# Performance work log

Hardware: AMD Instinct MI355X
Metric: run time of the kernel (lower is better)

The kernel has to match this reference:

```python
import jax, jax.numpy as jnp
import numpy as np

N = 50000
E = 800000
DIM = 256
HEADS = 4
HDIM = DIM // HEADS  # 64
NEG_SLOPE = 0.2
LN_EPS = 1e-5


def _layernorm(x, g, b):
    mu = jnp.mean(x, axis=-1, keepdims=True)
    var = jnp.var(x, axis=-1, keepdims=True)
    return (x - mu) * jax.lax.rsqrt(var + LN_EPS) * g + b


def setup_inputs() -> dict:
    key = jax.random.key(0)
    ks = jax.random.split(key, 10)
    x = jax.random.normal(ks[0], (N, DIM), dtype=jnp.float32)
    edge_index = jax.random.randint(ks[1], (2, E), 0, N, dtype=jnp.int64)
    s = 0.05
    W = jax.random.normal(ks[2], (DIM, DIM), dtype=jnp.float32) * s       # GAT linear (heads*out = dim)
    a_src = jax.random.normal(ks[3], (HEADS, HDIM), dtype=jnp.float32) * s
    a_dst = jax.random.normal(ks[4], (HEADS, HDIM), dtype=jnp.float32) * s
    gat_b = jnp.zeros((DIM,), dtype=jnp.float32)
    ln_g = jnp.ones((DIM,), dtype=jnp.float32)
    ln_b = jnp.zeros((DIM,), dtype=jnp.float32)
    W1 = jax.random.normal(ks[5], (DIM, 4 * DIM), dtype=jnp.float32) * s
    b1 = jnp.zeros((4 * DIM,), dtype=jnp.float32)
    W2 = jax.random.normal(ks[6], (4 * DIM, DIM), dtype=jnp.float32) * s
    b2 = jnp.zeros((DIM,), dtype=jnp.float32)
    return {"x": x, "edge_index": edge_index, "W": W, "a_src": a_src,
            "a_dst": a_dst, "gat_b": gat_b, "ln_g": ln_g, "ln_b": ln_b,
            "W1": W1, "b1": b1, "W2": W2, "b2": b2}


def _gat(x, edge_index, W, a_src, a_dst, gat_b):
    # project and split heads: [N, H, C]
    h = (x @ W).reshape(N, HEADS, HDIM)
    alpha_src = jnp.einsum('nhc,hc->nh', h, a_src)  # [N, H]
    alpha_dst = jnp.einsum('nhc,hc->nh', h, a_dst)  # [N, H]
    src = edge_index[0]
    dst = edge_index[1]
    e = jax.nn.leaky_relu(alpha_src[src] + alpha_dst[dst], NEG_SLOPE)  # [E, H]
    # segment softmax over edges sharing a destination node
    m = jax.ops.segment_max(e, dst, num_segments=N)                   # [N, H]
    ex = jnp.exp(e - m[dst])
    denom = jax.ops.segment_sum(ex, dst, num_segments=N)              # [N, H]
    alpha = ex / (denom[dst] + 1e-16)                                 # [E, H]
    msg = h[src] * alpha[:, :, None]                                  # [E, H, C]
    out = jax.ops.segment_sum(msg.reshape(E, DIM), dst, num_segments=N)
    return out + gat_b


def reference(x, edge_index, W, a_src, a_dst, gat_b, ln_g, ln_b, W1, b1, W2, b2):
    residual = x
    g = _gat(x, edge_index, W, a_src, a_dst, gat_b)
    x = _layernorm(x + g, ln_g, ln_b)
    ffn = jax.nn.gelu(x @ W1 + b1, approximate=False) @ W2 + b2
    x = _layernorm(x + ffn, ln_g, ln_b)  # same norm params reused, as in source
    return x + residual
```

## Files before the change

kernel.cpp:

```cpp
#include <hip/hip_runtime.h>
#include <hip/hip_bf16.h>
#include <math.h>

typedef __bf16 bf16;
typedef bf16 bf16x8 __attribute__((ext_vector_type(8)));
typedef float floatx4 __attribute__((ext_vector_type(4)));

#define NN 50000
#define EE 800000
#define DIMC 256
#define FFC 1024

typedef __attribute__((address_space(3))) unsigned int lds_u32;
typedef __attribute__((address_space(1))) unsigned int gbl_u32;

static __device__ __forceinline__ void glds16(const bf16* g, bf16* l) {
    __builtin_amdgcn_global_load_lds((const gbl_u32*)g, (lds_u32*)l, 16, 0, 0);
}

static __device__ __forceinline__ unsigned short f2b(float f) {
    bf16 b = (bf16)f;
    return __builtin_bit_cast(unsigned short, b);
}
static __device__ __forceinline__ float b2f_lo(unsigned u) { return __uint_as_float(u << 16); }
static __device__ __forceinline__ float b2f_hi(unsigned u) { return __uint_as_float(u & 0xffff0000u); }

static __device__ __forceinline__ float gelu_f(float v) {
    float z = -1.5957691216f * v - 0.0713548163f * v * v * v;
    return v / (1.f + __expf(z));
}

__global__ __launch_bounds__(256)
void k_cast_count(const float* __restrict__ in, bf16* __restrict__ out, long n4,
                  const int* __restrict__ dst, unsigned* __restrict__ deg) {
    long i = (long)blockIdx.x * 256 + threadIdx.x;
    if (i < EE) atomicAdd(&deg[dst[(int)i]], 1u);
    if (i >= n4) return;
    float4 v = ((const float4*)in)[i];
    uint2 p;
    p.x = (unsigned)f2b(v.x) | ((unsigned)f2b(v.y) << 16);
    p.y = (unsigned)f2b(v.z) | ((unsigned)f2b(v.w) << 16);
    ((uint2*)out)[i] = p;
}

__global__ __launch_bounds__(256)
void k_tcast_all(const float* __restrict__ W, bf16* __restrict__ WT,
                 const float* __restrict__ W1, bf16* __restrict__ W1T,
                 const float* __restrict__ W2, bf16* __restrict__ W2T) {
    __shared__ float t[32][33];
    int b = blockIdx.x;
    const float* in; bf16* out; int K, Nc, bx, by;
    if (b < 64)        { in = W;  out = WT;  K = 256;  Nc = 256;  bx = b & 7;  by = b >> 3; }
    else if (b < 320)  { b -= 64;  in = W1; out = W1T; K = 256;  Nc = 1024; bx = b & 31; by = b >> 5; }
    else               { b -= 320; in = W2; out = W2T; K = 1024; Nc = 256;  bx = b & 7;  by = b >> 3; }
    int n0 = bx * 32, k0 = by * 32;
    int tx = threadIdx.x & 31, ty = threadIdx.x >> 5;
#pragma unroll
    for (int i = 0; i < 4; ++i)
        t[ty + i * 8][tx] = in[(long)(k0 + ty + i * 8) * Nc + n0 + tx];
    __syncthreads();
#pragma unroll
    for (int i = 0; i < 4; ++i)
        out[(long)(n0 + ty + i * 8) * K + k0 + tx] = (bf16)t[tx][ty + i * 8];
}

template <int EPI>
__global__ __launch_bounds__(256)
void k_gemmA(const bf16* __restrict__ A, const bf16* __restrict__ BT,
             bf16* __restrict__ C, const float* __restrict__ bias,
             const float* __restrict__ avs, const float* __restrict__ avd,
             float* __restrict__ asrcO, float* __restrict__ adstO,
             int M, int K, int Nc) {
    __shared__ __attribute__((aligned(16))) bf16 smem[17408];
    bf16* As = smem;
    bf16* Bs = smem + 8192;
    const int tid = threadIdx.x;
    const int w = tid >> 6, lane = tid & 63;
    const int gm = blockIdx.x * 128, gn = blockIdx.y * 128;
    const int wm = (w >> 1) * 64, wn = (w & 1) * 64;
    const int lr = lane & 15, lkc = lane >> 4;

    long aoff[4], boff[4];
#pragma unroll
    for (int j = 0; j < 4; ++j) {
        int s = w * 4 + j;
        int r = s * 8 + (lane >> 3);
        int kc = ((lane & 7) ^ (r & 7)) * 8;
        aoff[j] = (long)min(gm + r, M - 1) * K + kc;
        boff[j] = (long)(gn + r) * K + kc;
    }

    floatx4 acc[4][4];
#pragma unroll
    for (int a = 0; a < 4; ++a)
#pragma unroll
        for (int b = 0; b < 4; ++b) acc[a][b] = floatx4{0.f, 0.f, 0.f, 0.f};

    for (int k0 = 0; k0 < K; k0 += 64) {
        if (k0) __syncthreads();
#pragma unroll
        for (int j = 0; j < 4; ++j) {
            int s = w * 4 + j;
            glds16(A + aoff[j] + k0, As + s * 512);
            glds16(BT + boff[j] + k0, Bs + s * 512);
        }
        __syncthreads();
#pragma unroll
        for (int kk = 0; kk < 2; ++kk) {
            bf16x8 af[4], bv[4];
#pragma unroll
            for (int mi = 0; mi < 4; ++mi) {
                int r = wm + mi * 16 + lr;
                int ch = (kk * 4 + lkc) ^ (r & 7);
                af[mi] = *(const bf16x8*)(As + r * 64 + ch * 8);
            }
#pragma unroll
            for (int ni = 0; ni < 4; ++ni) {
                int r = wn + ni * 16 + lr;
                int ch = (kk * 4 + lkc) ^ (r & 7);
                bv[ni] = *(const bf16x8*)(Bs + r * 64 + ch * 8);
            }
#pragma unroll
            for (int mi = 0; mi < 4; ++mi)
#pragma unroll
                for (int ni = 0; ni < 4; ++ni)
                    acc[mi][ni] = __builtin_amdgcn_mfma_f32_16x16x32_bf16(af[mi], bv[ni], acc[mi][ni], 0, 0, 0);
        }
    }

    __syncthreads();
    bf16* cs = smem;
#pragma unroll
    for (int ni = 0; ni < 4; ++ni) {
        const int cl = wn + ni * 16 + lr;
        const float bvs = (EPI == 1) ? bias[gn + cl] : 0.f;
#pragma unroll
        for (int mi = 0; mi < 4; ++mi)
#pragma unroll
            for (int i = 0; i < 4; ++i) {
                int rl = wm + mi * 16 + lkc * 4 + i;
                float v = acc[mi][ni][i] + bvs;
                if (EPI == 1) v = gelu_f(v);
                cs[rl * 136 + cl] = (bf16)v;
            }
    }
    __syncthreads();

    const int c8 = (lane & 15) * 8;
    float as8[8], ad8[8];
    int hd = 0;
    if (EPI == 0) {
        hd = (gn >> 6) + ((lane & 15) >> 3);
        const int cb = hd * 64 + (c8 & 63);
#pragma unroll
        for (int i = 0; i < 8; ++i) { as8[i] = avs[cb + i]; ad8[i] = avd[cb + i]; }
    }

#pragma unroll
    for (int t = 0; t < 8; ++t) {
        int rl = w * 32 + t * 4 + (lane >> 4);
        int grow = gm + rl;
        uint4 val = *(const uint4*)(cs + rl * 136 + c8);
        if (grow < M) *(uint4*)(C + (long)grow * Nc + gn + c8) = val;
        if (EPI == 0) {
            float h0 = b2f_lo(val.x), h1 = b2f_hi(val.x), h2 = b2f_lo(val.y), h3 = b2f_hi(val.y);
            float h4 = b2f_lo(val.z), h5 = b2f_hi(val.z), h6 = b2f_lo(val.w), h7 = b2f_hi(val.w);
            float ds = h0 * as8[0] + h1 * as8[1] + h2 * as8[2] + h3 * as8[3]
                     + h4 * as8[4] + h5 * as8[5] + h6 * as8[6] + h7 * as8[7];
            float dd = h0 * ad8[0] + h1 * ad8[1] + h2 * ad8[2] + h3 * ad8[3]
                     + h4 * ad8[4] + h5 * ad8[5] + h6 * ad8[6] + h7 * ad8[7];
#pragma unroll
            for (int off = 1; off < 8; off <<= 1) { ds += __shfl_xor(ds, off); dd += __shfl_xor(dd, off); }
            if ((lane & 7) == 0 && grow < M) {
                asrcO[grow * 4 + hd] = ds;
                adstO[grow * 4 + hd] = dd;
            }
        }
    }
}

__global__ __launch_bounds__(512)
void k_ffn(const bf16* __restrict__ x1b, const bf16* __restrict__ W1T,
           const bf16* __restrict__ W2T, const float* __restrict__ b1,
           const float* __restrict__ b2, const float* __restrict__ x,
           const float* __restrict__ lng, const float* __restrict__ lnb,
           float* __restrict__ out, int M) {
    __shared__ __attribute__((aligned(16))) bf16 smem[20480];
    float* actf = (float*)smem;
    bf16* w1s = smem + 4096;
    bf16* w2s = smem + 12288;
    const int tid = threadIdx.x;
    const int w = tid >> 6, lane = tid & 63;
    const int lr = lane & 15, lkc = lane >> 4;
    const int mg = w >> 1, nh = w & 1;
    const int gm = blockIdx.x * 64;

    bf16x8 xf[8];
    {
        long rb = (long)min(gm + mg * 16 + lr, M - 1) * DIMC;
#pragma unroll
        for (int kf = 0; kf < 8; ++kf)
            xf[kf] = *(const bf16x8*)(x1b + rb + kf * 32 + lkc * 8);
    }

    floatx4 accB[8];
#pragma unroll
    for (int i = 0; i < 8; ++i) accB[i] = floatx4{0.f, 0.f, 0.f, 0.f};

    const int rbA = nh * 16 + lr;
    const int rAct = mg * 16 + lr;
    const int kAct = nh * 16 + lr;

    for (int c = 0; c < 32; ++c) {
        if (c) __syncthreads();
#pragma unroll
        for (int j = 0; j < 2; ++j) {
            int sg = w * 2 + j;
            int r = sg * 2 + (lane >> 5);
            int col = ((lane & 31) ^ (r & 7)) * 8;
            glds16(W1T + (long)(c * 32 + r) * DIMC + col, w1s + sg * 512);
        }
#pragma unroll
        for (int j = 0; j < 2; ++j) {
            int sg = w * 2 + j;
            int r = sg * 16 + (lane >> 2);
            int col = c * 32 + (((lane & 3) ^ ((r >> 1) & 3)) * 8);
            glds16(W2T + (long)r * FFC + col, w2s + sg * 512);
        }
        __syncthreads();

        floatx4 a0 = floatx4{0.f, 0.f, 0.f, 0.f}, a1 = a0;
#pragma unroll
        for (int kf = 0; kf < 8; kf += 2) {
            int g0 = (kf * 4 + lkc) ^ (rbA & 7);
            int g1 = ((kf + 1) * 4 + lkc) ^ (rbA & 7);
            bf16x8 bva = *(const bf16x8*)(w1s + rbA * 256 + g0 * 8);
            bf16x8 bvb = *(const bf16x8*)(w1s + rbA * 256 + g1 * 8);
            a0 = __builtin_amdgcn_mfma_f32_16x16x32_bf16(xf[kf], bva, a0, 0, 0, 0);
            a1 = __builtin_amdgcn_mfma_f32_16x16x32_bf16(xf[kf + 1], bvb, a1, 0, 0, 0);
        }
        float b1v = b1[c * 32 + kAct];
#pragma unroll
        for (int i = 0; i < 4; ++i) {
            int r = mg * 16 + lkc * 4 + i;
            float v = gelu_f(a0[i] + a1[i] + b1v);
            actf[r * 32 + (((kAct >> 2) ^ (r & 7)) << 2) + (kAct & 3)] = v;
        }
        __syncthreads();

        {
            int g0 = (lkc * 2) ^ (rAct & 7);
            int g1 = (lkc * 2 + 1) ^ (rAct & 7);
            float4 lo = *(const float4*)(actf + rAct * 32 + g0 * 4);
            float4 hi = *(const float4*)(actf + rAct * 32 + g1 * 4);
            bf16x8 af;
            af[0] = (bf16)lo.x; af[1] = (bf16)lo.y; af[2] = (bf16)lo.z; af[3] = (bf16)lo.w;
            af[4] = (bf16)hi.x; af[5] = (bf16)hi.y; af[6] = (bf16)hi.z; af[7] = (bf16)hi.w;
#pragma unroll
            for (int ni = 0; ni < 8; ++ni) {
                int rb = nh * 128 + ni * 16 + lr;
                int gb = lkc ^ ((rb >> 1) & 3);
                bf16x8 bv = *(const bf16x8*)(w2s + rb * 32 + gb * 8);
                accB[ni] = __builtin_amdgcn_mfma_f32_16x16x32_bf16(af, bv, accB[ni], 0, 0, 0);
            }
        }
    }

    __syncthreads();
    bf16* cs = smem;
#pragma unroll
    for (int ni = 0; ni < 8; ++ni) {
        int col = nh * 128 + ni * 16 + lr;
        float b2v = b2[col];
#pragma unroll
        for (int i = 0; i < 4; ++i) {
            int rl = mg * 16 + lkc * 4 + i;
            cs[rl * 264 + col] = (bf16)(accB[ni][i] + b2v);
        }
    }
    __syncthreads();
    float4 g4 = *(const float4*)(lng + lane * 4);
    float4 lb4 = *(const float4*)(lnb + lane * 4);
#pragma unroll 1
    for (int t = 0; t < 8; ++t) {
        int r = w * 8 + t;
        int grow = gm + r;
        long base = (long)min(grow, M - 1) * DIMC + lane * 4;
        uint2 cu = *(const uint2*)(cs + r * 264 + lane * 4);
        uint2 xu = *(const uint2*)(x1b + base);
        float v0 = b2f_lo(cu.x) + b2f_lo(xu.x);
        float v1 = b2f_hi(cu.x) + b2f_hi(xu.x);
        float v2 = b2f_lo(cu.y) + b2f_lo(xu.y);
        float v3 = b2f_hi(cu.y) + b2f_hi(xu.y);
        float s1 = v0 + v1 + v2 + v3;
        float s2 = v0 * v0 + v1 * v1 + v2 * v2 + v3 * v3;
#pragma unroll
        for (int off = 1; off < 64; off <<= 1) { s1 += __shfl_xor(s1, off); s2 += __shfl_xor(s2, off); }
        float mu = s1 * (1.f / DIMC);
        float rs = rsqrtf(s2 * (1.f / DIMC) - mu * mu + 1e-5f);
        float4 xr = *(const float4*)(x + base);
        float4 o;
        o.x = (v0 - mu) * rs * g4.x + lb4.x + xr.x;
        o.y = (v1 - mu) * rs * g4.y + lb4.y + xr.y;
        o.z = (v2 - mu) * rs * g4.z + lb4.z + xr.z;
        o.w = (v3 - mu) * rs * g4.w + lb4.w + xr.w;
        if (grow < M) *(float4*)(out + (long)grow * DIMC + lane * 4) = o;
    }
}

__global__ __launch_bounds__(1024)
void k_scan1(const unsigned* __restrict__ deg, unsigned* __restrict__ rowoff,
             unsigned* __restrict__ cursor, unsigned* __restrict__ bsum) {
    __shared__ unsigned wsum[16], wscan[16];
    int tid = threadIdx.x, lane = tid & 63, wid = tid >> 6;
    int i = blockIdx.x * 1024 + tid;
    unsigned v = (i < NN) ? deg[i] : 0u;
    unsigned s = v;
    for (int off = 1; off < 64; off <<= 1) {
        unsigned t = __shfl_up(s, off);
        if (lane >= off) s += t;
    }
    if (lane == 63) wsum[wid] = s;
    __syncthreads();
    if (wid == 0) {
        unsigned t = (lane < 16) ? wsum[lane] : 0u;
        unsigned ts = t;
        for (int off = 1; off < 16; off <<= 1) {
            unsigned u2 = __shfl_up(ts, off);
            if (lane >= off) ts += u2;
        }
        if (lane < 16) wscan[lane] = ts;
    }
    __syncthreads();
    unsigned basew = (wid > 0) ? wscan[wid - 1] : 0u;
    unsigned excl = basew + (s - v);
    if (i < NN) { rowoff[i] = excl; cursor[i] = excl; }
    if (tid == 0) bsum[blockIdx.x] = wscan[15];
}

__global__ __launch_bounds__(64)
void k_scan2(unsigned* __restrict__ bsum, unsigned* __restrict__ rowoff) {
    int lane = threadIdx.x;
    unsigned v = (lane < 49) ? bsum[lane] : 0u;
    unsigned s = v;
    for (int off = 1; off < 64; off <<= 1) {
        unsigned t = __shfl_up(s, off);
        if (lane >= off) s += t;
    }
    if (lane < 49) bsum[lane] = s - v;
    if (lane == 48) rowoff[NN] = s;
}

__global__ __launch_bounds__(256)
void k_scan3(const unsigned* __restrict__ bsum, unsigned* __restrict__ rowoff,
             unsigned* __restrict__ cursor) {
    int i = blockIdx.x * 256 + threadIdx.x;
    if (i < NN) {
        unsigned o = bsum[i >> 10];
        rowoff[i] += o;
        cursor[i] += o;
    }
}

__global__ __launch_bounds__(256)
void k_fill(const int* __restrict__ src, const int* __restrict__ dst,
            unsigned* __restrict__ cursor, unsigned* __restrict__ elist) {
    int e = blockIdx.x * 256 + threadIdx.x;
    if (e < EE) {
        unsigned p = atomicAdd(&cursor[dst[e]], 1u);
        elist[p] = (unsigned)src[e];
    }
}

__global__ __launch_bounds__(256)
void k_agg_ln1(const unsigned* __restrict__ rowoff, const unsigned* __restrict__ elist,
               const float* __restrict__ asrc, const float* __restrict__ adst,
               const bf16* __restrict__ hb, const float* __restrict__ x,
               const float* __restrict__ gatb, const float* __restrict__ lng,
               const float* __restrict__ lnb, bf16* __restrict__ x1b) {
    int node = (blockIdx.x * 256 + threadIdx.x) >> 6;
    int lane = threadIdx.x & 63;
    if (node >= NN) return;
    int beg = (int)rowoff[node], end = (int)rowoff[node + 1];
    int head = lane >> 4;
    float ad = adst[node * 4 + head];
    const int c = lane * 4;
    const bf16* hc = hb + c;
    const int bl = lane & 48;

    float dsum = 0.f;
    float a0 = 0.f, a1 = 0.f, a2 = 0.f, a3 = 0.f;

    for (int c0 = beg; c0 < end; c0 += 16) {
        int take = end - c0; if (take > 16) take = 16;
        int jj = c0 + (lane & 15);
        float ex = 0.f; int s = 0;
        if (jj < end) {
            s = (int)elist[jj];
            float e = asrc[s * 4 + head] + ad;
            e = (e > 0.f) ? e : 0.2f * e;
            ex = __expf(e);
        }
        dsum += ex;
        if (take == 16) {
#pragma unroll
            for (int j = 0; j < 16; ++j) {
                float al = __shfl(ex, bl + j);
                int sj = __shfl(s, bl + j);
                uint2 u = *(const uint2*)(hc + (long)sj * DIMC);
                a0 += al * b2f_lo(u.x);
                a1 += al * b2f_hi(u.x);
                a2 += al * b2f_lo(u.y);
                a3 += al * b2f_hi(u.y);
            }
        } else {
            for (int j = 0; j < take; ++j) {
                float al = __shfl(ex, bl + j);
                int sj = __shfl(s, bl + j);
                uint2 u = *(const uint2*)(hc + (long)sj * DIMC);
                a0 += al * b2f_lo(u.x);
                a1 += al * b2f_hi(u.x);
                a2 += al * b2f_lo(u.y);
                a3 += al * b2f_hi(u.y);
            }
        }
    }
    dsum += __shfl_xor(dsum, 1);
    dsum += __shfl_xor(dsum, 2);
    dsum += __shfl_xor(dsum, 4);
    dsum += __shfl_xor(dsum, 8);
    float invd = 1.f / (dsum + 1e-16f);
    a0 *= invd; a1 *= invd; a2 *= invd; a3 *= invd;

    long base = (long)node * DIMC + c;
    float4 xr = *(const float4*)(x + base);
    float4 gb = *(const float4*)(gatb + c);
    float v0 = xr.x + a0 + gb.x;
    float v1 = xr.y + a1 + gb.y;
    float v2 = xr.z + a2 + gb.z;
    float v3 = xr.w + a3 + gb.w;
    float s1 = v0 + v1 + v2 + v3;
    float s2 = v0 * v0 + v1 * v1 + v2 * v2 + v3 * v3;
    for (int off = 1; off < 64; off <<= 1) { s1 += __shfl_xor(s1, off); s2 += __shfl_xor(s2, off); }
    float mu = s1 * (1.f / DIMC);
    float rs = rsqrtf(s2 * (1.f / DIMC) - mu * mu + 1e-5f);
    float4 g4 = *(const float4*)(lng + c);
    float4 b4 = *(const float4*)(lnb + c);
    float y0 = (v0 - mu) * rs * g4.x + b4.x;
    float y1 = (v1 - mu) * rs * g4.y + b4.y;
    float y2 = (v2 - mu) * rs * g4.z + b4.z;
    float y3 = (v3 - mu) * rs * g4.w + b4.w;
    uint2 p;
    p.x = (unsigned)f2b(y0) | ((unsigned)f2b(y1) << 16);
    p.y = (unsigned)f2b(y2) | ((unsigned)f2b(y3) << 16);
    *(uint2*)(x1b + base) = p;
}

extern "C" void kernel_launch(void* const* d_in, const int* in_sizes, int n_in,
                              void* d_out, int out_size, void* d_ws, size_t ws_size,
                              hipStream_t stream) {
    const float* x    = (const float*)d_in[0];
    const int*   ei   = (const int*)d_in[1];
    const float* W    = (const float*)d_in[2];
    const float* a_s  = (const float*)d_in[3];
    const float* a_d  = (const float*)d_in[4];
    const float* gatb = (const float*)d_in[5];
    const float* lng  = (const float*)d_in[6];
    const float* lnb  = (const float*)d_in[7];
    const float* W1   = (const float*)d_in[8];
    const float* b1   = (const float*)d_in[9];
    const float* W2   = (const float*)d_in[10];
    const float* b2   = (const float*)d_in[11];
    float* out = (float*)d_out;
    char* ws = (char*)d_ws;

    bf16*     xb     = (bf16*)(ws + 0L);
    bf16*     hb     = (bf16*)(ws + 25600000L);
    bf16*     x1b    = (bf16*)(ws + 51200000L);
    unsigned* bsum   = (unsigned*)(ws + 76800000L);
    float*    asrc   = (float*)(ws + 179200000L);
    float*    adst   = (float*)(ws + 180000000L);
    unsigned* deg    = (unsigned*)(ws + 180800000L);
    unsigned* cursor = (unsigned*)(ws + 181000192L);
    unsigned* rowoff = (unsigned*)(ws + 181200384L);
    unsigned* elist  = (unsigned*)(ws + 181400832L);
    bf16*     WT     = (bf16*)(ws + 184600832L);
    bf16*     W1T    = (bf16*)(ws + 184731904L);
    bf16*     W2T    = (bf16*)(ws + 185256192L);

    const int* esrc = ei;
    const int* edst = ei + EE;

    hipMemsetAsync(deg, 0, NN * sizeof(unsigned), stream);
    k_cast_count<<<12500, 256, 0, stream>>>(x, xb, (long)NN * DIMC / 4, edst, deg);
    k_tcast_all<<<576, 256, 0, stream>>>(W, WT, W1, W1T, W2, W2T);

    dim3 g1(391, 2);
    k_gemmA<0><<<g1, 256, 0, stream>>>(xb, WT, hb, nullptr, a_s, a_d, asrc, adst, NN, DIMC, DIMC);

    k_scan1<<<49, 1024, 0, stream>>>(deg, rowoff, cursor, bsum);
    k_scan2<<<1, 64, 0, stream>>>(bsum, rowoff);
    k_scan3<<<196, 256, 0, stream>>>(bsum, rowoff, cursor);
    k_fill<<<3125, 256, 0, stream>>>(esrc, edst, cursor, elist);

    k_agg_ln1<<<12500, 256, 0, stream>>>(rowoff, elist, asrc, adst, hb, x, gatb, lng, lnb, x1b);

    k_ffn<<<782, 512, 0, stream>>>(x1b, W1T, W2T, b1, b2, x, lng, lnb, out, NN);
}
```

Before: 442.2 us.

## Double-buffer FFN weight staging and pre-gather source attention scores in CSR fill

The FFN kernel now double-buffers the W1/W2 chunk staging in LDS. It prefetches chunk c+1 with async global-to-LDS loads while computing chunk c, and swaps the second __syncthreads for a waitcnt plus raw barrier. Separately, k_fill writes each edge's four source attention scores into a CSR-ordered float4 array, so the aggregation kernel reads them contiguously instead of gathering asrc by random source index. The costs are more LDS per block (which may lower occupancy of the 512-thread FFN blocks) and an extra 12.8 MB scattered write in k_fill.

```diff
diff --git a/kernel.cpp b/kernel.cpp
--- a/kernel.cpp
+++ b/kernel.cpp
@@ -179,16 +179,33 @@
     }
 }
 
+#define STAGE_W(cc, pp) do {                                                    \
+    bf16* w1d = smem + 4096 + (pp) * 8192;                                      \
+    bf16* w2d = smem + 20480 + (pp) * 8192;                                     \
+    _Pragma("unroll")                                                           \
+    for (int j = 0; j < 2; ++j) {                                               \
+        int sg = w * 2 + j;                                                     \
+        int r = sg * 2 + (lane >> 5);                                           \
+        int col = ((lane & 31) ^ (r & 7)) * 8;                                  \
+        glds16(W1T + (long)((cc) * 32 + r) * DIMC + col, w1d + sg * 512);       \
+    }                                                                           \
+    _Pragma("unroll")                                                           \
+    for (int j = 0; j < 2; ++j) {                                               \
+        int sg = w * 2 + j;                                                     \
+        int r = sg * 16 + (lane >> 2);                                          \
+        int col = (cc) * 32 + (((lane & 3) ^ ((r >> 1) & 3)) * 8);              \
+        glds16(W2T + (long)r * FFC + col, w2d + sg * 512);                      \
+    }                                                                           \
+} while (0)
+
 __global__ __launch_bounds__(512)
 void k_ffn(const bf16* __restrict__ x1b, const bf16* __restrict__ W1T,
            const bf16* __restrict__ W2T, const float* __restrict__ b1,
            const float* __restrict__ b2, const float* __restrict__ x,
            const float* __restrict__ lng, const float* __restrict__ lnb,
            float* __restrict__ out, int M) {
-    __shared__ __attribute__((aligned(16))) bf16 smem[20480];
+    __shared__ __attribute__((aligned(16))) bf16 smem[36864];
     float* actf = (float*)smem;
-    bf16* w1s = smem + 4096;
-    bf16* w2s = smem + 12288;
     const int tid = threadIdx.x;
     const int w = tid >> 6, lane = tid & 63;
     const int lr = lane & 15, lkc = lane >> 4;
@@ -211,23 +228,14 @@
     const int rAct = mg * 16 + lr;
     const int kAct = nh * 16 + lr;
 
+    STAGE_W(0, 0);
+
     for (int c = 0; c < 32; ++c) {
-        if (c) __syncthreads();
-#pragma unroll
-        for (int j = 0; j < 2; ++j) {
-            int sg = w * 2 + j;
-            int r = sg * 2 + (lane >> 5);
-            int col = ((lane & 31) ^ (r & 7)) * 8;
-            glds16(W1T + (long)(c * 32 + r) * DIMC + col, w1s + sg * 512);
-        }
-#pragma unroll
-        for (int j = 0; j < 2; ++j) {
-            int sg = w * 2 + j;
-            int r = sg * 16 + (lane >> 2);
-            int col = c * 32 + (((lane & 3) ^ ((r >> 1) & 3)) * 8);
-            glds16(W2T + (long)r * FFC + col, w2s + sg * 512);
-        }
+        const int p = c & 1;
         __syncthreads();
+        if (c < 31) STAGE_W(c + 1, p ^ 1);
+        bf16* w1s = smem + 4096 + p * 8192;
+        bf16* w2s = smem + 20480 + p * 8192;
 
         floatx4 a0 = floatx4{0.f, 0.f, 0.f, 0.f}, a1 = a0;
 #pragma unroll
@@ -246,7 +254,9 @@
             float v = gelu_f(a0[i] + a1[i] + b1v);
             actf[r * 32 + (((kAct >> 2) ^ (r & 7)) << 2) + (kAct & 3)] = v;
         }
-        __syncthreads();
+        asm volatile("s_waitcnt lgkmcnt(0)" ::: "memory");
+        __builtin_amdgcn_s_barrier();
+        asm volatile("" ::: "memory");
 
         {
             int g0 = (lkc * 2) ^ (rAct & 7);
@@ -364,17 +374,20 @@
 
 __global__ __launch_bounds__(256)
 void k_fill(const int* __restrict__ src, const int* __restrict__ dst,
-            unsigned* __restrict__ cursor, unsigned* __restrict__ elist) {
+            const float* __restrict__ asrc, unsigned* __restrict__ cursor,
+            unsigned* __restrict__ elist, float4* __restrict__ evals) {
     int e = blockIdx.x * 256 + threadIdx.x;
     if (e < EE) {
+        int s = src[e];
         unsigned p = atomicAdd(&cursor[dst[e]], 1u);
-        elist[p] = (unsigned)src[e];
+        elist[p] = (unsigned)s;
+        evals[p] = *(const float4*)(asrc + (long)s * 4);
     }
 }
 
 __global__ __launch_bounds__(256)
 void k_agg_ln1(const unsigned* __restrict__ rowoff, const unsigned* __restrict__ elist,
-               const float* __restrict__ asrc, const float* __restrict__ adst,
+               const float* __restrict__ evals, const float* __restrict__ adst,
                const bf16* __restrict__ hb, const float* __restrict__ x,
                const float* __restrict__ gatb, const float* __restrict__ lng,
                const float* __restrict__ lnb, bf16* __restrict__ x1b) {
@@ -397,7 +410,7 @@
         float ex = 0.f; int s = 0;
         if (jj < end) {
             s = (int)elist[jj];
-            float e = asrc[s * 4 + head] + ad;
+            float e = evals[(long)jj * 4 + head] + ad;
             e = (e > 0.f) ? e : 0.2f * e;
             ex = __expf(e);
         }
@@ -478,6 +491,7 @@
     bf16*     hb     = (bf16*)(ws + 25600000L);
     bf16*     x1b    = (bf16*)(ws + 51200000L);
     unsigned* bsum   = (unsigned*)(ws + 76800000L);
+    float4*   evals  = (float4*)(ws + 77000032L);
     float*    asrc   = (float*)(ws + 179200000L);
     float*    adst   = (float*)(ws + 180000000L);
     unsigned* deg    = (unsigned*)(ws + 180800000L);
@@ -501,9 +515,9 @@
     k_scan1<<<49, 1024, 0, stream>>>(deg, rowoff, cursor, bsum);
     k_scan2<<<1, 64, 0, stream>>>(bsum, rowoff);
     k_scan3<<<196, 256, 0, stream>>>(bsum, rowoff, cursor);
-    k_fill<<<3125, 256, 0, stream>>>(esrc, edst, cursor, elist);
-
-    k_agg_ln1<<<12500, 256, 0, stream>>>(rowoff, elist, asrc, adst, hb, x, gatb, lng, lnb, x1b);
+    k_fill<<<3125, 256, 0, stream>>>(esrc, edst, asrc, cursor, elist, evals);
+
+    k_agg_ln1<<<12500, 256, 0, stream>>>(rowoff, elist, (const float*)evals, adst, hb, x, gatb, lng, lnb, x1b);
 
     k_ffn<<<782, 512, 0, stream>>>(x1b, W1T, W2T, b1, b2, x, lng, lnb, out, NN);
 }
```

After: 441.7 us. About the same (-0.1%).
